# Performance work log

Measured on AMD Instinct MI355X. Metric: run time of the kernel, lower is better.

## Reference

```python
import jax, jax.numpy as jnp
import numpy as np

C_IN, C_OUT, K = 2048, 1024, 2  # k=2 -> 5x5 correlation window
B, H, W = 4, 64, 64


def conv1x1(x, w, b):
    # x: [B,C,H,W], w: [O,C], b: [O]
    return jnp.einsum('bchw,oc->bohw', x, w) + b[None, :, None, None]


def bn_star(x, Kstd=3.0):
    # torch.std is unbiased (ddof=1); clip outliers above mu+K*std to 1
    mu = jnp.mean(x, axis=0, keepdims=True)
    std = jnp.std(x, axis=0, ddof=1, keepdims=True)
    lim = mu + Kstd * std
    return jnp.where(x > lim, jnp.float32(1.0), x)


def match_trans(curr_F, prev_F, prev_M):
    # curr_F/prev_F: [B,2048,H,W]; prev_M: [B,1024,H,W]
    b, c, h, w = prev_F.shape
    prev_nc = jnp.sum(prev_F, axis=1)  # [B,H,W]
    curr_nc = jnp.sum(curr_F, axis=1)  # [B,H,W]
    pad_nc = jnp.pad(prev_nc, ((0, 0), (K, K), (K, K)))
    pad_M = jnp.pad(prev_M, ((0, 0), (0, 0), (K, K), (K, K)))
    # shifted copies: shift(i,j)(y,x) = prev_nc_padded(y-i, x-j)
    shifts = jnp.stack([pad_nc[:, K - i:K - i + h, K - j:K - j + w]
                        for i in range(-K, K + 1) for j in range(-K, K + 1)], axis=0)  # [25,B,H,W]
    # sum_filter(prev_F) summed over channels == C * 5x5 local sum of prev_nc
    denom = curr_nc * (jnp.float32(c) * jnp.sum(shifts, axis=0))  # [B,H,W]
    aligned = jnp.zeros_like(prev_M)
    idx = 0
    for i in range(-K, K + 1):
        for j in range(-K, K + 1):
            mask_ij = curr_nc * shifts[idx] / denom  # [B,H,W]
            aligned = aligned + mask_ij[:, None] * pad_M[:, :, K - i:K - i + h, K - j:K - j + w]
            idx += 1
    return aligned


def setup_inputs() -> dict:
    key = jax.random.key(0)
    ks = jax.random.split(key, 16)
    s = jnp.float32(0.02)
    inp = {
        'curr_F': jax.random.uniform(ks[0], (B, C_IN, H, W), jnp.float32),
        'prev_F': jax.random.uniform(ks[1], (B, C_IN, H, W), jnp.float32),
        'prev_M': jax.random.normal(ks[2], (B, C_OUT, H, W), jnp.float32),
        'Wz_w': jax.random.normal(ks[3], (C_OUT, C_IN), jnp.float32) * s,
        'Wz_b': jnp.zeros((C_OUT,), jnp.float32),
        'Wr_w': jax.random.normal(ks[4], (C_OUT, C_IN), jnp.float32) * s,
        'Wr_b': jnp.zeros((C_OUT,), jnp.float32),
        'W_w': jax.random.normal(ks[5], (C_OUT, C_IN), jnp.float32) * s,
        'W_b': jnp.zeros((C_OUT,), jnp.float32),
        'Uz_w': jax.random.normal(ks[6], (C_OUT, C_OUT), jnp.float32) * s,
        'Uz_b': jnp.zeros((C_OUT,), jnp.float32),
        'Ur_w': jax.random.normal(ks[7], (C_OUT, C_OUT), jnp.float32) * s,
        'Ur_b': jnp.zeros((C_OUT,), jnp.float32),
        'U_w': jax.random.normal(ks[8], (C_OUT, C_OUT), jnp.float32) * s,
        'U_b': jnp.zeros((C_OUT,), jnp.float32),
        'body': 1,
    }
    return inp


def reference(curr_F, prev_F, prev_M, Wz_w, Wz_b, Wr_w, Wr_b, W_w, W_b,
              Uz_w, Uz_b, Ur_w, Ur_b, U_w, U_b, body):
    if body:
        aligned = match_trans(curr_F, prev_F, prev_M)
    else:
        aligned = prev_M
    zt = bn_star(jax.nn.relu(conv1x1(curr_F, Wz_w, Wz_b) + conv1x1(aligned, Uz_w, Uz_b)))
    rt = bn_star(jax.nn.relu(conv1x1(curr_F, Wr_w, Wr_b) + conv1x1(aligned, Ur_w, Ur_b)))
    M = jax.nn.relu(conv1x1(curr_F, W_w, W_b) + conv1x1(aligned * rt, U_w, U_b))
    curr_M = (1.0 - zt) * aligned + zt * M
    return curr_M
```

## Files before the change

kernel.cpp:

```cpp
#include <hip/hip_runtime.h>
#include <hip/hip_bf16.h>

namespace {

constexpr int NB = 4;
constexpr int CI = 2048;
constexpr int CO = 1024;
constexpr int HW = 4096;
constexpr int MTOT = NB * HW;

typedef __attribute__((ext_vector_type(8))) short bf16x8;
typedef __attribute__((ext_vector_type(4))) float f32x4;
typedef __hip_bfloat16 bf16;

__device__ __forceinline__ void g2l16(void* lds, const void* g) {
  __builtin_amdgcn_global_load_lds((const __attribute__((address_space(1))) void*)g,
                                   (__attribute__((address_space(3))) void*)lds,
                                   16, 0, 0);
}

__global__ void zero_k(float* __restrict__ p, int n) {
  int i = blockIdx.x * 256 + threadIdx.x;
  if (i < n) p[i] = 0.f;
}

__global__ void castw6_k(const float* s0, const float* s1, const float* s2,
                         const float* s3, const float* s4, const float* s5,
                         bf16* d0, bf16* d1, bf16* d2, bf16* d3, bf16* d4, bf16* d5) {
  int y = blockIdx.y;
  const float* s = (y == 0) ? s0 : (y == 1) ? s1 : (y == 2) ? s2 : (y == 3) ? s3 : (y == 4) ? s4 : s5;
  bf16* d = (y == 0) ? d0 : (y == 1) ? d1 : (y == 2) ? d2 : (y == 3) ? d3 : (y == 4) ? d4 : d5;
  int n4 = ((y < 3) ? CI * CO : CO * CO) >> 2;
  int i = blockIdx.x * 256 + threadIdx.x;
  if (i < n4) {
    float4 v = ((const float4*)s)[i];
    union { ushort4 u; bf16 h[4]; } pk;
    pk.h[0] = __float2bfloat16(v.x);
    pk.h[1] = __float2bfloat16(v.y);
    pk.h[2] = __float2bfloat16(v.z);
    pk.h[3] = __float2bfloat16(v.w);
    ((ushort4*)d)[i] = pk.u;
  }
}

__global__ void nc_sum_k(const float* __restrict__ src, float* __restrict__ dst) {
  int p = blockIdx.x * 256 + threadIdx.x;
  int c0 = blockIdx.y * 128;
  int b = blockIdx.z;
  const float* s = src + ((long)b * CI + c0) * HW + p;
  float a = 0.f;
  #pragma unroll 8
  for (int c = 0; c < 128; ++c) a += s[(long)c * HW];
  atomicAdd(dst + b * HW + p, a);
}

template <typename T> __device__ __forceinline__ T cvt_out(float v);
template <> __device__ __forceinline__ float cvt_out<float>(float v) { return v; }
template <> __device__ __forceinline__ bf16 cvt_out<bf16>(float v) { return __float2bfloat16(v); }

template <typename TO>
__global__ void transpose_k(const float* __restrict__ src, TO* __restrict__ dst, int R, int S) {
  __shared__ float tile[32][33];
  int b = blockIdx.z;
  int r0 = blockIdx.x * 32, s0 = blockIdx.y * 32;
  int ts = threadIdx.x & 31, tr = threadIdx.x >> 5;
  const float* sp = src + ((long)b * R + r0) * S + s0;
  #pragma unroll
  for (int i = 0; i < 32; i += 8) tile[tr + i][ts] = sp[(long)(tr + i) * S + ts];
  __syncthreads();
  TO* dp = dst + ((long)b * S + s0) * R + r0;
  #pragma unroll
  for (int i = 0; i < 32; i += 8) dp[(long)(tr + i) * R + ts] = cvt_out<TO>(tile[ts][tr + i]);
}

__global__ void boxinv_k(const float* __restrict__ nc, float* __restrict__ invden) {
  int i = blockIdx.x * 256 + threadIdx.x;
  int b = i >> 12, p = i & 4095;
  int y = p >> 6, x = p & 63;
  float s = 0.f;
  #pragma unroll
  for (int dy = -2; dy <= 2; ++dy) {
    int yy = y + dy;
    if ((unsigned)yy >= 64u) continue;
    #pragma unroll
    for (int dx = -2; dx <= 2; ++dx) {
      int xx = x + dx;
      if ((unsigned)xx >= 64u) continue;
      s += nc[b * HW + yy * 64 + xx];
    }
  }
  invden[i] = 1.f / (2048.f * s);
}

__global__ void align_k(const float* __restrict__ pmcl, const float* __restrict__ nc,
                        const float* __restrict__ invden, const int* __restrict__ body,
                        bf16* __restrict__ ah) {
  int bp = blockIdx.x;
  int b = bp >> 12, p = bp & 4095;
  int y = p >> 6, x = p & 63;
  int c = threadIdx.x * 4;
  float4 acc = make_float4(0.f, 0.f, 0.f, 0.f);
  if (body[0]) {
    #pragma unroll
    for (int dy = -2; dy <= 2; ++dy) {
      int yy = y + dy;
      if ((unsigned)yy >= 64u) continue;
      #pragma unroll
      for (int dx = -2; dx <= 2; ++dx) {
        int xx = x + dx;
        if ((unsigned)xx >= 64u) continue;
        int sp = yy * 64 + xx;
        float w = nc[b * HW + sp];
        float4 v = *(const float4*)(pmcl + ((long)b * HW + sp) * CO + c);
        acc.x += w * v.x; acc.y += w * v.y; acc.z += w * v.z; acc.w += w * v.w;
      }
    }
    float s = invden[bp];
    acc.x *= s; acc.y *= s; acc.z *= s; acc.w *= s;
  } else {
    acc = *(const float4*)(pmcl + (long)bp * CO + c);
  }
  union { ushort4 u; bf16 h[4]; } pk;
  pk.h[0] = __float2bfloat16(acc.x);
  pk.h[1] = __float2bfloat16(acc.y);
  pk.h[2] = __float2bfloat16(acc.z);
  pk.h[3] = __float2bfloat16(acc.w);
  *(ushort4*)(ah + (long)bp * CO + c) = pk.u;
}

template <int MODE>
__global__ __launch_bounds__(512, 2) void gemm256(
    const bf16* __restrict__ A1, const bf16* __restrict__ B1,
    const bf16* __restrict__ A2, const bf16* __restrict__ B2,
    const float* __restrict__ bias1, const float* __restrict__ bias2,
    const float* __restrict__ ztp, const bf16* __restrict__ aligh,
    float* __restrict__ outf, bf16* __restrict__ outh,
    float* __restrict__ outcf) {
  constexpr int NT1 = CI / 32;
  constexpr int NT = NT1 + CO / 32;
  __shared__ __align__(16) char lds[131072];
  const int t = threadIdx.x, lane = t & 63, wid = t >> 6;
  const int wm = wid >> 2, wn = wid & 3;
  const int m0 = blockIdx.x * 256, n0 = blockIdx.y * 256;
  const int fr = lane & 15, kq = lane >> 4;

  const int b0i = (wid << 7) + lane;
  const int line0 = b0i >> 3;
  const int c3 = (b0i & 7) ^ (line0 & 7);
  const int row0 = 2 * line0 + (c3 >> 2);
  const int k16 = c3 & 3;
  const char* pa1 = (const char*)A1 + (((size_t)(m0 + row0) * CI + k16 * 8) << 1);
  const char* pa1h = pa1 + ((size_t)CI << 5);
  const char* pb1 = (const char*)B1 + (((size_t)(n0 + row0) * CI + k16 * 8) << 1);
  const char* pb1h = pb1 + ((size_t)CI << 5);
  const char* pa2 = (const char*)A2 + (((size_t)(m0 + row0) * CO + k16 * 8) << 1);
  const char* pa2h = pa2 + ((size_t)CO << 5);
  const char* pb2 = (const char*)B2 + (((size_t)(n0 + row0) * CO + k16 * 8) << 1);
  const char* pb2h = pb2 + ((size_t)CO << 5);

  auto STAGE = [&](int s) {
    const char *sa, *sah, *sb, *sbh;
    if (s < NT1) {
      size_t so = (size_t)s << 6;
      sa = pa1 + so; sah = pa1h + so; sb = pb1 + so; sbh = pb1h + so;
    } else {
      size_t so = (size_t)(s - NT1) << 6;
      sa = pa2 + so; sah = pa2h + so; sb = pb2 + so; sbh = pb2h + so;
    }
    char* d = lds + ((s & 3) << 15) + (wid << 11) + (lane << 4);
    g2l16(d, sa);
    g2l16(d + 1024, sah);
    g2l16(d + 16384, sb);
    g2l16(d + 17408, sbh);
  };

  int offA[8], offB[4];
  #pragma unroll
  for (int mi = 0; mi < 8; ++mi) {
    int r = (wm << 7) + (mi << 4) + fr;
    int ln = r >> 1;
    int cc = ((r & 1) << 2) | kq;
    offA[mi] = (ln << 7) + ((cc ^ (ln & 7)) << 4);
  }
  #pragma unroll
  for (int ni = 0; ni < 4; ++ni) {
    int r = (wn << 6) + (ni << 4) + fr;
    int ln = r >> 1;
    int cc = ((r & 1) << 2) | kq;
    offB[ni] = 16384 + (ln << 7) + ((cc ^ (ln & 7)) << 4);
  }

  f32x4 acc[8][4] = {};

  STAGE(0); STAGE(1); STAGE(2);

  auto PHASE = [&](int tp, int W, bool dostage) {
    if (dostage) STAGE(tp + 3);
    if (W == 12)      asm volatile("s_waitcnt vmcnt(12)" ::: "memory");
    else if (W == 8)  asm volatile("s_waitcnt vmcnt(8)" ::: "memory");
    else if (W == 4)  asm volatile("s_waitcnt vmcnt(4)" ::: "memory");
    else              asm volatile("s_waitcnt vmcnt(0)" ::: "memory");
    __builtin_amdgcn_s_barrier();
    asm volatile("" ::: "memory");
    const char* buf = lds + ((tp & 3) << 15);
    bf16x8 av[8], bv[4];
    #pragma unroll
    for (int mi = 0; mi < 8; ++mi) av[mi] = *(const bf16x8*)(buf + offA[mi]);
    #pragma unroll
    for (int ni = 0; ni < 4; ++ni) bv[ni] = *(const bf16x8*)(buf + offB[ni]);
    __builtin_amdgcn_s_setprio(1);
    #pragma unroll
    for (int mi = 0; mi < 8; ++mi)
      #pragma unroll
      for (int ni = 0; ni < 4; ++ni)
        acc[mi][ni] = __builtin_amdgcn_mfma_f32_16x16x32_bf16(av[mi], bv[ni], acc[mi][ni], 0, 0, 0);
    __builtin_amdgcn_s_setprio(0);
    asm volatile("" ::: "memory");
    __builtin_amdgcn_s_barrier();
  };

  #pragma unroll 1
  for (int tt = 0; tt < NT - 3; ++tt) PHASE(tt, 12, true);
  PHASE(NT - 3, 8, false);
  PHASE(NT - 2, 4, false);
  PHASE(NT - 1, 0, false);

  #pragma unroll
  for (int mi = 0; mi < 8; ++mi) {
    const int r0 = m0 + (wm << 7) + (mi << 4) + (kq << 2);
    #pragma unroll
    for (int ni = 0; ni < 4; ++ni) {
      const int col = n0 + (wn << 6) + (ni << 4) + fr;
      const float bsum = bias1[col] + bias2[col];
      if (MODE == 2) {
        const int bb = r0 >> 12, p0 = r0 & 4095;
        float4 o;
        float* po = &o.x;
        #pragma unroll
        for (int j = 0; j < 4; ++j) {
          const size_t idx = (size_t)(r0 + j) * CO + col;
          float m = fmaxf(acc[mi][ni][j] + bsum, 0.f);
          float z = ztp[idx];
          float a = __bfloat162float(aligh[idx]);
          po[j] = (1.f - z) * a + z * m;
        }
        *(float4*)(outcf + ((size_t)bb * CO + col) * HW + p0) = o;
      } else {
        #pragma unroll
        for (int j = 0; j < 4; ++j) {
          const size_t idx = (size_t)(r0 + j) * CO + col;
          float v = acc[mi][ni][j] + bsum;
          if (MODE == 0) {
            outf[idx] = fmaxf(v, 0.f);
          } else {
            float rt = fmaxf(v, 0.f);
            outh[idx] = __float2bfloat16(__bfloat162float(aligh[idx]) * rt);
          }
        }
      }
    }
  }
}

}

extern "C" void kernel_launch(void* const* d_in, const int* in_sizes, int n_in,
                              void* d_out, int out_size, void* d_ws, size_t ws_size,
                              hipStream_t stream) {
  const float* curr_F = (const float*)d_in[0];
  const float* prev_F = (const float*)d_in[1];
  const float* prev_M = (const float*)d_in[2];
  const float* Wz_w = (const float*)d_in[3];
  const float* Wz_b = (const float*)d_in[4];
  const float* Wr_w = (const float*)d_in[5];
  const float* Wr_b = (const float*)d_in[6];
  const float* W_w  = (const float*)d_in[7];
  const float* W_b  = (const float*)d_in[8];
  const float* Uz_w = (const float*)d_in[9];
  const float* Uz_b = (const float*)d_in[10];
  const float* Ur_w = (const float*)d_in[11];
  const float* Ur_b = (const float*)d_in[12];
  const float* U_w  = (const float*)d_in[13];
  const float* U_b  = (const float*)d_in[14];
  const int* body   = (const int*)d_in[15];
  float* out = (float*)d_out;

  char* ws = (char*)d_ws;
  const size_t M64 = 1ull << 26;
  const size_t M32 = 1ull << 25;
  bf16*  currF_h   = (bf16*)(ws);
  float* prevM_cl  = (float*)(ws + M64);
  float* zt        = (float*)(ws + M64);
  bf16*  align_h   = (bf16*)(ws + 2 * M64);
  bf16*  ar_h      = (bf16*)(ws + 2 * M64 + M32);
  char*  wb        = ws + 2 * M64 + 2 * M32;
  bf16* Wz_h = (bf16*)wb;
  bf16* Wr_h = Wz_h + (size_t)CO * CI;
  bf16* W_h  = Wr_h + (size_t)CO * CI;
  bf16* Uz_h = W_h  + (size_t)CO * CI;
  bf16* Ur_h = Uz_h + (size_t)CO * CO;
  bf16* U_h  = Ur_h + (size_t)CO * CO;
  float* prev_nc = (float*)(U_h + (size_t)CO * CO);
  float* invden  = prev_nc + NB * HW;

  castw6_k<<<dim3((CI * CO) / 1024, 6), 256, 0, stream>>>(
      Wz_w, Wr_w, W_w, Uz_w, Ur_w, U_w, Wz_h, Wr_h, W_h, Uz_h, Ur_h, U_h);

  zero_k<<<dim3((NB * HW) / 256), 256, 0, stream>>>(prev_nc, NB * HW);
  nc_sum_k<<<dim3(HW / 256, CI / 128, NB), 256, 0, stream>>>(prev_F, prev_nc);

  transpose_k<bf16><<<dim3(CI / 32, HW / 32, NB), 256, 0, stream>>>(curr_F, currF_h, CI, HW);
  transpose_k<float><<<dim3(CO / 32, HW / 32, NB), 256, 0, stream>>>(prev_M, prevM_cl, CO, HW);

  boxinv_k<<<dim3((NB * HW) / 256), 256, 0, stream>>>(prev_nc, invden);
  align_k<<<dim3(NB * HW), 256, 0, stream>>>(prevM_cl, prev_nc, invden, body, align_h);

  dim3 gg(MTOT / 256, CO / 256);
  gemm256<0><<<gg, 512, 0, stream>>>(currF_h, Wz_h, align_h, Uz_h,
                                     Wz_b, Uz_b, nullptr, nullptr, zt, nullptr, nullptr);
  gemm256<3><<<gg, 512, 0, stream>>>(currF_h, Wr_h, align_h, Ur_h,
                                     Wr_b, Ur_b, nullptr, align_h, nullptr, ar_h, nullptr);
  gemm256<2><<<gg, 512, 0, stream>>>(currF_h, W_h, ar_h, U_h,
                                     W_b, U_b, zt, align_h, nullptr, nullptr, out);
}
```

Baseline: 554.5 us.

## Shrink GEMM tiles to 128x128, store zt in bf16, vectorize transposes

Replaces the 256x256, 512-thread, 4-stage GEMM with a 128x128, 256-thread kernel that double-buffers 32 KB of LDS. This is meant to raise occupancy and spread the 16K x 1K output over more blocks. The zt intermediate is now stored in bf16 instead of fp32, which halves its write and read traffic at some cost in precision. The transpose kernels move to 64x64 tiles with float4 loads and stores. The smaller tiles lower data reuse per block and the shallower pipeline may hide less memory latency.

```diff
diff --git a/kernel.cpp b/kernel.cpp
--- a/kernel.cpp
+++ b/kernel.cpp
@@ -54,23 +54,44 @@
   atomicAdd(dst + b * HW + p, a);
 }
 
-template <typename T> __device__ __forceinline__ T cvt_out(float v);
-template <> __device__ __forceinline__ float cvt_out<float>(float v) { return v; }
-template <> __device__ __forceinline__ bf16 cvt_out<bf16>(float v) { return __float2bfloat16(v); }
-
 template <typename TO>
-__global__ void transpose_k(const float* __restrict__ src, TO* __restrict__ dst, int R, int S) {
-  __shared__ float tile[32][33];
-  int b = blockIdx.z;
-  int r0 = blockIdx.x * 32, s0 = blockIdx.y * 32;
-  int ts = threadIdx.x & 31, tr = threadIdx.x >> 5;
-  const float* sp = src + ((long)b * R + r0) * S + s0;
-  #pragma unroll
-  for (int i = 0; i < 32; i += 8) tile[tr + i][ts] = sp[(long)(tr + i) * S + ts];
+__global__ void transpose64_k(const float* __restrict__ src, TO* __restrict__ dst,
+                              int R, int S) {
+  __shared__ float tile[64][65];
+  const int b = blockIdx.z;
+  const int r0 = blockIdx.x * 64, s0 = blockIdx.y * 64;
+  const int t = threadIdx.x;
+  const int fc = t & 15;
+  const int rr = t >> 4;
+  const float* sp = src + ((size_t)b * R + r0) * S + s0;
+  #pragma unroll
+  for (int i = 0; i < 4; ++i) {
+    float4 v = *(const float4*)(sp + (size_t)(rr + i * 16) * S + fc * 4);
+    tile[rr + i * 16][fc * 4 + 0] = v.x;
+    tile[rr + i * 16][fc * 4 + 1] = v.y;
+    tile[rr + i * 16][fc * 4 + 2] = v.z;
+    tile[rr + i * 16][fc * 4 + 3] = v.w;
+  }
   __syncthreads();
-  TO* dp = dst + ((long)b * S + s0) * R + r0;
-  #pragma unroll
-  for (int i = 0; i < 32; i += 8) dp[(long)(tr + i) * R + ts] = cvt_out<TO>(tile[ts][tr + i]);
+  #pragma unroll
+  for (int i = 0; i < 4; ++i) {
+    const int sr = rr + i * 16;
+    float4 w;
+    w.x = tile[fc * 4 + 0][sr];
+    w.y = tile[fc * 4 + 1][sr];
+    w.z = tile[fc * 4 + 2][sr];
+    w.w = tile[fc * 4 + 3][sr];
+    if constexpr (sizeof(TO) == 4) {
+      *(float4*)((float*)dst + ((size_t)b * S + s0 + sr) * R + r0 + fc * 4) = w;
+    } else {
+      union { ushort4 u; bf16 h[4]; } pk;
+      pk.h[0] = __float2bfloat16(w.x);
+      pk.h[1] = __float2bfloat16(w.y);
+      pk.h[2] = __float2bfloat16(w.z);
+      pk.h[3] = __float2bfloat16(w.w);
+      *(ushort4*)((bf16*)dst + ((size_t)b * S + s0 + sr) * R + r0 + fc * 4) = pk.u;
+    }
+  }
 }
 
 __global__ void boxinv_k(const float* __restrict__ nc, float* __restrict__ invden) {
@@ -129,108 +150,97 @@
 }
 
 template <int MODE>
-__global__ __launch_bounds__(512, 2) void gemm256(
+__global__ __launch_bounds__(256, 4) void gemm128(
     const bf16* __restrict__ A1, const bf16* __restrict__ B1,
     const bf16* __restrict__ A2, const bf16* __restrict__ B2,
     const float* __restrict__ bias1, const float* __restrict__ bias2,
-    const float* __restrict__ ztp, const bf16* __restrict__ aligh,
-    float* __restrict__ outf, bf16* __restrict__ outh,
-    float* __restrict__ outcf) {
+    const bf16* __restrict__ ztp, const bf16* __restrict__ aligh,
+    bf16* __restrict__ outh, float* __restrict__ outcf) {
   constexpr int NT1 = CI / 32;
   constexpr int NT = NT1 + CO / 32;
-  __shared__ __align__(16) char lds[131072];
+  __shared__ __align__(16) char lds[32768];
   const int t = threadIdx.x, lane = t & 63, wid = t >> 6;
-  const int wm = wid >> 2, wn = wid & 3;
-  const int m0 = blockIdx.x * 256, n0 = blockIdx.y * 256;
+  const int wr = (wid >> 1) * 64, wc = (wid & 1) * 64;
+  const int m0 = blockIdx.x * 128, n0 = blockIdx.y * 128;
   const int fr = lane & 15, kq = lane >> 4;
 
-  const int b0i = (wid << 7) + lane;
-  const int line0 = b0i >> 3;
-  const int c3 = (b0i & 7) ^ (line0 & 7);
-  const int row0 = 2 * line0 + (c3 >> 2);
-  const int k16 = c3 & 3;
+  const int line0 = t >> 3;
+  const int cc = (t & 7) ^ (line0 & 7);
+  const int row0 = 2 * line0 + (cc >> 2);
+  const int k16 = cc & 3;
   const char* pa1 = (const char*)A1 + (((size_t)(m0 + row0) * CI + k16 * 8) << 1);
-  const char* pa1h = pa1 + ((size_t)CI << 5);
   const char* pb1 = (const char*)B1 + (((size_t)(n0 + row0) * CI + k16 * 8) << 1);
-  const char* pb1h = pb1 + ((size_t)CI << 5);
   const char* pa2 = (const char*)A2 + (((size_t)(m0 + row0) * CO + k16 * 8) << 1);
-  const char* pa2h = pa2 + ((size_t)CO << 5);
   const char* pb2 = (const char*)B2 + (((size_t)(n0 + row0) * CO + k16 * 8) << 1);
-  const char* pb2h = pb2 + ((size_t)CO << 5);
 
   auto STAGE = [&](int s) {
     const char *sa, *sah, *sb, *sbh;
     if (s < NT1) {
       size_t so = (size_t)s << 6;
-      sa = pa1 + so; sah = pa1h + so; sb = pb1 + so; sbh = pb1h + so;
+      sa = pa1 + so; sah = sa + ((size_t)CI << 7);
+      sb = pb1 + so; sbh = sb + ((size_t)CI << 7);
     } else {
       size_t so = (size_t)(s - NT1) << 6;
-      sa = pa2 + so; sah = pa2h + so; sb = pb2 + so; sbh = pb2h + so;
-    }
-    char* d = lds + ((s & 3) << 15) + (wid << 11) + (lane << 4);
+      sa = pa2 + so; sah = sa + ((size_t)CO << 7);
+      sb = pb2 + so; sbh = sb + ((size_t)CO << 7);
+    }
+    char* d = lds + ((s & 1) << 14) + (t << 4);
     g2l16(d, sa);
-    g2l16(d + 1024, sah);
-    g2l16(d + 16384, sb);
-    g2l16(d + 17408, sbh);
+    g2l16(d + 4096, sah);
+    g2l16(d + 8192, sb);
+    g2l16(d + 12288, sbh);
   };
 
-  int offA[8], offB[4];
-  #pragma unroll
-  for (int mi = 0; mi < 8; ++mi) {
-    int r = (wm << 7) + (mi << 4) + fr;
+  int offA[4], offB[4];
+  #pragma unroll
+  for (int i = 0; i < 4; ++i) {
+    int r = wr + i * 16 + fr;
     int ln = r >> 1;
-    int cc = ((r & 1) << 2) | kq;
-    offA[mi] = (ln << 7) + ((cc ^ (ln & 7)) << 4);
-  }
-  #pragma unroll
-  for (int ni = 0; ni < 4; ++ni) {
-    int r = (wn << 6) + (ni << 4) + fr;
-    int ln = r >> 1;
-    int cc = ((r & 1) << 2) | kq;
-    offB[ni] = 16384 + (ln << 7) + ((cc ^ (ln & 7)) << 4);
-  }
-
-  f32x4 acc[8][4] = {};
-
-  STAGE(0); STAGE(1); STAGE(2);
-
-  auto PHASE = [&](int tp, int W, bool dostage) {
-    if (dostage) STAGE(tp + 3);
-    if (W == 12)      asm volatile("s_waitcnt vmcnt(12)" ::: "memory");
-    else if (W == 8)  asm volatile("s_waitcnt vmcnt(8)" ::: "memory");
-    else if (W == 4)  asm volatile("s_waitcnt vmcnt(4)" ::: "memory");
-    else              asm volatile("s_waitcnt vmcnt(0)" ::: "memory");
+    int c = ((r & 1) << 2) | kq;
+    offA[i] = (ln << 7) + ((c ^ (ln & 7)) << 4);
+    r = wc + i * 16 + fr;
+    ln = r >> 1;
+    c = ((r & 1) << 2) | kq;
+    offB[i] = 8192 + (ln << 7) + ((c ^ (ln & 7)) << 4);
+  }
+
+  f32x4 acc[4][4] = {};
+
+  STAGE(0);
+
+  #pragma unroll 1
+  for (int s = 0; s < NT; ++s) {
+    if (s + 1 < NT) {
+      STAGE(s + 1);
+      asm volatile("s_waitcnt vmcnt(4)" ::: "memory");
+    } else {
+      asm volatile("s_waitcnt vmcnt(0)" ::: "memory");
+    }
     __builtin_amdgcn_s_barrier();
     asm volatile("" ::: "memory");
-    const char* buf = lds + ((tp & 3) << 15);
-    bf16x8 av[8], bv[4];
-    #pragma unroll
-    for (int mi = 0; mi < 8; ++mi) av[mi] = *(const bf16x8*)(buf + offA[mi]);
-    #pragma unroll
-    for (int ni = 0; ni < 4; ++ni) bv[ni] = *(const bf16x8*)(buf + offB[ni]);
+    const char* buf = lds + ((s & 1) << 14);
+    bf16x8 av[4], bv[4];
+    #pragma unroll
+    for (int i = 0; i < 4; ++i) av[i] = *(const bf16x8*)(buf + offA[i]);
+    #pragma unroll
+    for (int i = 0; i < 4; ++i) bv[i] = *(const bf16x8*)(buf + offB[i]);
     __builtin_amdgcn_s_setprio(1);
     #pragma unroll
-    for (int mi = 0; mi < 8; ++mi)
+    for (int mi = 0; mi < 4; ++mi)
       #pragma unroll
       for (int ni = 0; ni < 4; ++ni)
         acc[mi][ni] = __builtin_amdgcn_mfma_f32_16x16x32_bf16(av[mi], bv[ni], acc[mi][ni], 0, 0, 0);
     __builtin_amdgcn_s_setprio(0);
     asm volatile("" ::: "memory");
     __builtin_amdgcn_s_barrier();
-  };
-
-  #pragma unroll 1
-  for (int tt = 0; tt < NT - 3; ++tt) PHASE(tt, 12, true);
-  PHASE(NT - 3, 8, false);
-  PHASE(NT - 2, 4, false);
-  PHASE(NT - 1, 0, false);
-
-  #pragma unroll
-  for (int mi = 0; mi < 8; ++mi) {
-    const int r0 = m0 + (wm << 7) + (mi << 4) + (kq << 2);
+  }
+
+  #pragma unroll
+  for (int mi = 0; mi < 4; ++mi) {
+    const int r0 = m0 + wr + mi * 16 + kq * 4;
     #pragma unroll
     for (int ni = 0; ni < 4; ++ni) {
-      const int col = n0 + (wn << 6) + (ni << 4) + fr;
+      const int col = n0 + wc + ni * 16 + fr;
       const float bsum = bias1[col] + bias2[col];
       if (MODE == 2) {
         const int bb = r0 >> 12, p0 = r0 & 4095;
@@ -240,7 +250,7 @@
         for (int j = 0; j < 4; ++j) {
           const size_t idx = (size_t)(r0 + j) * CO + col;
           float m = fmaxf(acc[mi][ni][j] + bsum, 0.f);
-          float z = ztp[idx];
+          float z = __bfloat162float(ztp[idx]);
           float a = __bfloat162float(aligh[idx]);
           po[j] = (1.f - z) * a + z * m;
         }
@@ -251,7 +261,7 @@
           const size_t idx = (size_t)(r0 + j) * CO + col;
           float v = acc[mi][ni][j] + bsum;
           if (MODE == 0) {
-            outf[idx] = fmaxf(v, 0.f);
+            outh[idx] = __float2bfloat16(fmaxf(v, 0.f));
           } else {
             float rt = fmaxf(v, 0.f);
             outh[idx] = __float2bfloat16(__bfloat162float(aligh[idx]) * rt);
@@ -290,7 +300,7 @@
   const size_t M32 = 1ull << 25;
   bf16*  currF_h   = (bf16*)(ws);
   float* prevM_cl  = (float*)(ws + M64);
-  float* zt        = (float*)(ws + M64);
+  bf16*  zt        = (bf16*)(ws + M64);
   bf16*  align_h   = (bf16*)(ws + 2 * M64);
   bf16*  ar_h      = (bf16*)(ws + 2 * M64 + M32);
   char*  wb        = ws + 2 * M64 + 2 * M32;
@@ -309,17 +319,17 @@
   zero_k<<<dim3((NB * HW) / 256), 256, 0, stream>>>(prev_nc, NB * HW);
   nc_sum_k<<<dim3(HW / 256, CI / 128, NB), 256, 0, stream>>>(prev_F, prev_nc);
 
-  transpose_k<bf16><<<dim3(CI / 32, HW / 32, NB), 256, 0, stream>>>(curr_F, currF_h, CI, HW);
-  transpose_k<float><<<dim3(CO / 32, HW / 32, NB), 256, 0, stream>>>(prev_M, prevM_cl, CO, HW);
+  transpose64_k<bf16><<<dim3(CI / 64, HW / 64, NB), 256, 0, stream>>>(curr_F, currF_h, CI, HW);
+  transpose64_k<float><<<dim3(CO / 64, HW / 64, NB), 256, 0, stream>>>(prev_M, prevM_cl, CO, HW);
 
   boxinv_k<<<dim3((NB * HW) / 256), 256, 0, stream>>>(prev_nc, invden);
   align_k<<<dim3(NB * HW), 256, 0, stream>>>(prevM_cl, prev_nc, invden, body, align_h);
 
-  dim3 gg(MTOT / 256, CO / 256);
-  gemm256<0><<<gg, 512, 0, stream>>>(currF_h, Wz_h, align_h, Uz_h,
-                                     Wz_b, Uz_b, nullptr, nullptr, zt, nullptr, nullptr);
-  gemm256<3><<<gg, 512, 0, stream>>>(currF_h, Wr_h, align_h, Ur_h,
-                                     Wr_b, Ur_b, nullptr, align_h, nullptr, ar_h, nullptr);
-  gemm256<2><<<gg, 512, 0, stream>>>(currF_h, W_h, ar_h, U_h,
-                                     W_b, U_b, zt, align_h, nullptr, nullptr, out);
-}
+  dim3 gg(MTOT / 128, CO / 128);
+  gemm128<0><<<gg, 256, 0, stream>>>(currF_h, Wz_h, align_h, Uz_h,
+                                     Wz_b, Uz_b, nullptr, nullptr, zt, nullptr);
+  gemm128<3><<<gg, 256, 0, stream>>>(currF_h, Wr_h, align_h, Ur_h,
+                                     Wr_b, Ur_b, nullptr, align_h, ar_h, nullptr);
+  gemm128<2><<<gg, 256, 0, stream>>>(currF_h, W_h, ar_h, U_h,
+                                     W_b, U_b, zt, align_h, nullptr, out);
+}
```

Result: slower. 622.9 us (+12.3%).

## Vectorize transposes with 64x64 tiles, store zt as bf16, swap GEMM grid order

Applied to the files above, without the earlier changes.

Replaces the 32x32 scalar transpose with a 64x64-tile transpose that uses float4 loads and vectorized stores. The zt intermediate is now written and read as bf16 instead of fp32, which halves that traffic but adds rounding before the final blend. The GEMM grid is reordered so consecutive blocks share the same A rows across N tiles, aiming for better L2 reuse of the activations.

```diff
diff --git a/kernel.cpp b/kernel.cpp
--- a/kernel.cpp
+++ b/kernel.cpp
@@ -54,23 +54,44 @@
   atomicAdd(dst + b * HW + p, a);
 }
 
-template <typename T> __device__ __forceinline__ T cvt_out(float v);
-template <> __device__ __forceinline__ float cvt_out<float>(float v) { return v; }
-template <> __device__ __forceinline__ bf16 cvt_out<bf16>(float v) { return __float2bfloat16(v); }
-
 template <typename TO>
-__global__ void transpose_k(const float* __restrict__ src, TO* __restrict__ dst, int R, int S) {
-  __shared__ float tile[32][33];
-  int b = blockIdx.z;
-  int r0 = blockIdx.x * 32, s0 = blockIdx.y * 32;
-  int ts = threadIdx.x & 31, tr = threadIdx.x >> 5;
-  const float* sp = src + ((long)b * R + r0) * S + s0;
-  #pragma unroll
-  for (int i = 0; i < 32; i += 8) tile[tr + i][ts] = sp[(long)(tr + i) * S + ts];
+__global__ void transpose64_k(const float* __restrict__ src, TO* __restrict__ dst,
+                              int R, int S) {
+  __shared__ float tile[64][65];
+  const int b = blockIdx.z;
+  const int r0 = blockIdx.x * 64, s0 = blockIdx.y * 64;
+  const int t = threadIdx.x;
+  const int fc = t & 15;
+  const int rr = t >> 4;
+  const float* sp = src + ((size_t)b * R + r0) * S + s0;
+  #pragma unroll
+  for (int i = 0; i < 4; ++i) {
+    float4 v = *(const float4*)(sp + (size_t)(rr + i * 16) * S + fc * 4);
+    tile[rr + i * 16][fc * 4 + 0] = v.x;
+    tile[rr + i * 16][fc * 4 + 1] = v.y;
+    tile[rr + i * 16][fc * 4 + 2] = v.z;
+    tile[rr + i * 16][fc * 4 + 3] = v.w;
+  }
   __syncthreads();
-  TO* dp = dst + ((long)b * S + s0) * R + r0;
-  #pragma unroll
-  for (int i = 0; i < 32; i += 8) dp[(long)(tr + i) * R + ts] = cvt_out<TO>(tile[ts][tr + i]);
+  #pragma unroll
+  for (int i = 0; i < 4; ++i) {
+    const int sr = rr + i * 16;
+    float4 w;
+    w.x = tile[fc * 4 + 0][sr];
+    w.y = tile[fc * 4 + 1][sr];
+    w.z = tile[fc * 4 + 2][sr];
+    w.w = tile[fc * 4 + 3][sr];
+    if constexpr (sizeof(TO) == 4) {
+      *(float4*)((float*)dst + ((size_t)b * S + s0 + sr) * R + r0 + fc * 4) = w;
+    } else {
+      union { ushort4 u; bf16 h[4]; } pk;
+      pk.h[0] = __float2bfloat16(w.x);
+      pk.h[1] = __float2bfloat16(w.y);
+      pk.h[2] = __float2bfloat16(w.z);
+      pk.h[3] = __float2bfloat16(w.w);
+      *(ushort4*)((bf16*)dst + ((size_t)b * S + s0 + sr) * R + r0 + fc * 4) = pk.u;
+    }
+  }
 }
 
 __global__ void boxinv_k(const float* __restrict__ nc, float* __restrict__ invden) {
@@ -133,15 +154,14 @@
     const bf16* __restrict__ A1, const bf16* __restrict__ B1,
     const bf16* __restrict__ A2, const bf16* __restrict__ B2,
     const float* __restrict__ bias1, const float* __restrict__ bias2,
-    const float* __restrict__ ztp, const bf16* __restrict__ aligh,
-    float* __restrict__ outf, bf16* __restrict__ outh,
-    float* __restrict__ outcf) {
+    const bf16* __restrict__ ztp, const bf16* __restrict__ aligh,
+    bf16* __restrict__ outh, float* __restrict__ outcf) {
   constexpr int NT1 = CI / 32;
   constexpr int NT = NT1 + CO / 32;
   __shared__ __align__(16) char lds[131072];
   const int t = threadIdx.x, lane = t & 63, wid = t >> 6;
   const int wm = wid >> 2, wn = wid & 3;
-  const int m0 = blockIdx.x * 256, n0 = blockIdx.y * 256;
+  const int m0 = blockIdx.y * 256, n0 = blockIdx.x * 256;
   const int fr = lane & 15, kq = lane >> 4;
 
   const int b0i = (wid << 7) + lane;
@@ -240,7 +260,7 @@
         for (int j = 0; j < 4; ++j) {
           const size_t idx = (size_t)(r0 + j) * CO + col;
           float m = fmaxf(acc[mi][ni][j] + bsum, 0.f);
-          float z = ztp[idx];
+          float z = __bfloat162float(ztp[idx]);
           float a = __bfloat162float(aligh[idx]);
           po[j] = (1.f - z) * a + z * m;
         }
@@ -251,7 +271,7 @@
           const size_t idx = (size_t)(r0 + j) * CO + col;
           float v = acc[mi][ni][j] + bsum;
           if (MODE == 0) {
-            outf[idx] = fmaxf(v, 0.f);
+            outh[idx] = __float2bfloat16(fmaxf(v, 0.f));
           } else {
             float rt = fmaxf(v, 0.f);
             outh[idx] = __float2bfloat16(__bfloat162float(aligh[idx]) * rt);
@@ -290,7 +310,7 @@
   const size_t M32 = 1ull << 25;
   bf16*  currF_h   = (bf16*)(ws);
   float* prevM_cl  = (float*)(ws + M64);
-  float* zt        = (float*)(ws + M64);
+  bf16*  zt        = (bf16*)(ws + M64);
   bf16*  align_h   = (bf16*)(ws + 2 * M64);
   bf16*  ar_h      = (bf16*)(ws + 2 * M64 + M32);
   char*  wb        = ws + 2 * M64 + 2 * M32;
@@ -309,17 +329,17 @@
   zero_k<<<dim3((NB * HW) / 256), 256, 0, stream>>>(prev_nc, NB * HW);
   nc_sum_k<<<dim3(HW / 256, CI / 128, NB), 256, 0, stream>>>(prev_F, prev_nc);
 
-  transpose_k<bf16><<<dim3(CI / 32, HW / 32, NB), 256, 0, stream>>>(curr_F, currF_h, CI, HW);
-  transpose_k<float><<<dim3(CO / 32, HW / 32, NB), 256, 0, stream>>>(prev_M, prevM_cl, CO, HW);
+  transpose64_k<bf16><<<dim3(CI / 64, HW / 64, NB), 256, 0, stream>>>(curr_F, currF_h, CI, HW);
+  transpose64_k<float><<<dim3(CO / 64, HW / 64, NB), 256, 0, stream>>>(prev_M, prevM_cl, CO, HW);
 
   boxinv_k<<<dim3((NB * HW) / 256), 256, 0, stream>>>(prev_nc, invden);
   align_k<<<dim3(NB * HW), 256, 0, stream>>>(prevM_cl, prev_nc, invden, body, align_h);
 
-  dim3 gg(MTOT / 256, CO / 256);
+  dim3 gg(CO / 256, MTOT / 256);
   gemm256<0><<<gg, 512, 0, stream>>>(currF_h, Wz_h, align_h, Uz_h,
-                                     Wz_b, Uz_b, nullptr, nullptr, zt, nullptr, nullptr);
+                                     Wz_b, Uz_b, nullptr, nullptr, zt, nullptr);
   gemm256<3><<<gg, 512, 0, stream>>>(currF_h, Wr_h, align_h, Ur_h,
-                                     Wr_b, Ur_b, nullptr, align_h, nullptr, ar_h, nullptr);
+                                     Wr_b, Ur_b, nullptr, align_h, ar_h, nullptr);
   gemm256<2><<<gg, 512, 0, stream>>>(currF_h, W_h, ar_h, U_h,
-                                     W_b, U_b, zt, align_h, nullptr, nullptr, out);
-}
+                                     W_b, U_b, zt, align_h, nullptr, out);
+}
```

Result: slower. 580.3 us (+4.7%).
